# Kernel tuning notes

Hardware: AMD Instinct MI355X
Metric: run time of the kernel (lower is better)

The kernel has to match this reference:

```python
import jax, jax.numpy as jnp
import numpy as np

N_NODES = 100000
N_EDGES = 1600000
IN_F = 64
HID = 64
OUT_F = 64


def _param(key, shape, fan_in):
    return jax.random.normal(key, shape, dtype=jnp.float32) * (1.0 / np.sqrt(fan_in))


def setup_inputs() -> dict:
    key = jax.random.key(0)
    ks = jax.random.split(key, 12)
    features = jax.random.normal(ks[0], (N_NODES, IN_F), dtype=jnp.float32)
    src = jax.random.randint(ks[1], (N_EDGES,), 0, N_NODES, dtype=jnp.int32)
    dst = jax.random.randint(ks[2], (N_EDGES,), 0, N_NODES, dtype=jnp.int32)
    dims = [(IN_F, HID), (HID, HID), (HID, OUT_F)]
    inp = {"features": features, "src": src, "dst": dst}
    for i, (din, dout) in enumerate(dims):
        inp[f"W_self{i}"] = _param(ks[3 + 3 * i], (din, dout), din)
        inp[f"W_neigh{i}"] = _param(ks[4 + 3 * i], (din, dout), din)
        inp[f"b{i}"] = jnp.zeros((dout,), dtype=jnp.float32)
    return inp


def _sage_layer(h, src, dst, W_self, W_neigh, b, deg_inv, n_nodes, act):
    # mean aggregation over in-neighbors: gather src feats, segment-sum into dst
    msum = jax.ops.segment_sum(h[src], dst, num_segments=n_nodes)  # [N, d]
    h_neigh = msum * deg_inv  # mean (zero-degree nodes -> 0, matching DGL)
    out = h @ W_self + h_neigh @ W_neigh + b
    return jax.nn.relu(out) if act else out


def reference(features, src, dst, W_self0, W_neigh0, b0, W_self1, W_neigh1, b1, W_self2, W_neigh2, b2):
    n = features.shape[0]
    deg = jax.ops.segment_sum(jnp.ones((src.shape[0],), jnp.float32), dst, num_segments=n)
    deg_inv = (1.0 / jnp.maximum(deg, 1.0))[:, None]  # [N, 1]
    h = _sage_layer(features, src, dst, W_self0, W_neigh0, b0, deg_inv, n, act=True)
    h = _sage_layer(h, src, dst, W_self1, W_neigh1, b1, deg_inv, n, act=True)
    h = _sage_layer(h, src, dst, W_self2, W_neigh2, b2, deg_inv, n, act=False)
    return h
```

## Files before the change

### kernel.cpp

```cpp
#include <hip/hip_runtime.h>

#define NF 64
#define BUCKET 128
#define MAXB 8192
#define EPB 4096

typedef __attribute__((ext_vector_type(8))) short bf16x8;
typedef __attribute__((ext_vector_type(4))) float f32x4;
typedef __attribute__((ext_vector_type(4))) unsigned int u32x4;

__device__ __forceinline__ float bf2f(unsigned short x) {
    union { unsigned int u; float f; } v; v.u = ((unsigned int)x) << 16; return v.f;
}
__device__ __forceinline__ unsigned short f2bf(float x) {
    union { float f; unsigned int u; } v; v.f = x;
    unsigned int r = (v.u + 0x7FFFu + ((v.u >> 16) & 1u)) >> 16;
    return (unsigned short)r;
}


__global__ __launch_bounds__(256) void bhist_kernel(const int* __restrict__ dst,
                                                    int* __restrict__ bins,
                                                    int n_edges, int nb) {
    __shared__ int h[MAXB];
    for (int i = threadIdx.x; i < nb; i += 256) h[i] = 0;
    __syncthreads();
    int base = blockIdx.x * EPB;
    int lim = min(base + EPB, n_edges);
    for (int i = base + threadIdx.x; i < lim; i += 256)
        atomicAdd(&h[dst[i] >> 7], 1);
    __syncthreads();
    for (int i = threadIdx.x; i < nb; i += 256) {
        int v = h[i];
        if (v) atomicAdd(&bins[i], v);
    }
}

__global__ __launch_bounds__(1024) void bscan_kernel(const int* __restrict__ bins,
                                                     int* __restrict__ bptr,
                                                     int* __restrict__ gcur, int nb) {
    __shared__ int sd[1024];
    int carry = 0;
    if (threadIdx.x == 0) bptr[0] = 0;
    for (int base = 0; base < nb; base += 1024) {
        int i = base + threadIdx.x;
        int v = (i < nb) ? bins[i] : 0;
        sd[threadIdx.x] = v;
        __syncthreads();
        for (int off = 1; off < 1024; off <<= 1) {
            int t = (threadIdx.x >= off) ? sd[threadIdx.x - off] : 0;
            __syncthreads();
            sd[threadIdx.x] += t;
            __syncthreads();
        }
        if (i < nb) {
            int ex = carry + sd[threadIdx.x] - v;
            bptr[i + 1] = carry + sd[threadIdx.x];
            gcur[i] = ex;
        }
        int last = sd[1023];
        __syncthreads();
        carry += last;
    }
}

__global__ __launch_bounds__(256) void bscatter_kernel(const int* __restrict__ src,
                                                       const int* __restrict__ dst,
                                                       int* __restrict__ gcur,
                                                       unsigned* __restrict__ bedges,
                                                       int n_edges, int nb) {
    __shared__ int h[MAXB];
    for (int i = threadIdx.x; i < nb; i += 256) h[i] = 0;
    __syncthreads();
    int base = blockIdx.x * EPB;
    int myDst[16], mySrc[16];
#pragma unroll
    for (int k = 0; k < 16; ++k) {
        int i = base + k * 256 + threadIdx.x;
        if (i < n_edges) {
            myDst[k] = dst[i];
            mySrc[k] = src[i];
            atomicAdd(&h[myDst[k] >> 7], 1);
        } else {
            myDst[k] = -1;
        }
    }
    __syncthreads();
    for (int i = threadIdx.x; i < nb; i += 256) {
        int v = h[i];
        h[i] = v ? atomicAdd(&gcur[i], v) : 0;
    }
    __syncthreads();
#pragma unroll
    for (int k = 0; k < 16; ++k) {
        if (myDst[k] >= 0) {
            int bin = myDst[k] >> 7;
            int pos = atomicAdd(&h[bin], 1);
            bedges[pos] = ((unsigned)mySrc[k] << 7) | (unsigned)(myDst[k] & 127);
        }
    }
}

__global__ __launch_bounds__(256) void bfinal_kernel(
    const unsigned* __restrict__ bedges, const int* __restrict__ bptr,
    int* __restrict__ row_ptr, int* __restrict__ col,
    int n_nodes, int n_edges, int nb) {
    __shared__ int cnt[BUCKET];
    __shared__ int sa[BUCKET], sb2[BUCKET];
    int tid = threadIdx.x;
    int b = blockIdx.x;
    int beg = bptr[b], end = bptr[b + 1];
    if (tid < BUCKET) cnt[tid] = 0;
    __syncthreads();
    for (int i = beg + tid; i < end; i += 256)
        atomicAdd(&cnt[bedges[i] & (BUCKET - 1)], 1);
    __syncthreads();
    if (tid < BUCKET) sa[tid] = cnt[tid];
    __syncthreads();
    int* pin = sa; int* pout = sb2;
    for (int off = 1; off < BUCKET; off <<= 1) {
        if (tid < BUCKET) pout[tid] = pin[tid] + ((tid >= off) ? pin[tid - off] : 0);
        __syncthreads();
        int* t = pin; pin = pout; pout = t;
    }
    int nodeBase = b * BUCKET;
    if (tid < BUCKET && nodeBase + tid < n_nodes)
        row_ptr[nodeBase + tid] = beg + (tid ? pin[tid - 1] : 0);
    if (b == nb - 1 && tid == 0) row_ptr[n_nodes] = n_edges;
    __syncthreads();
    if (tid < BUCKET) cnt[tid] = 0;
    __syncthreads();
    for (int i = beg + tid; i < end; i += 256) {
        unsigned e = bedges[i];
        int d = e & (BUCKET - 1);
        int pos = beg + (d ? pin[d - 1] : 0) + atomicAdd(&cnt[d], 1);
        col[pos] = (int)(e >> 7);
    }
}


__global__ void convert_kernel(const float* __restrict__ in, unsigned short* __restrict__ X, int n_nodes) {
    int t = blockIdx.x * blockDim.x + threadIdx.x;
    int total = n_nodes * 16;
    if (t >= total) return;
    int n = t >> 4, g = t & 15;
    float4 v = *reinterpret_cast<const float4*>(in + (size_t)n * 64 + g * 4);
    ushort4 o;
    o.x = f2bf(v.x); o.y = f2bf(v.y); o.z = f2bf(v.z); o.w = f2bf(v.w);
    *reinterpret_cast<ushort4*>(X + (size_t)n * 128 + g * 4) = o;
}

__global__ void wtrans_kernel(const float* __restrict__ Ws0, const float* __restrict__ Wn0,
                              const float* __restrict__ Ws1, const float* __restrict__ Wn1,
                              const float* __restrict__ Ws2, const float* __restrict__ Wn2,
                              unsigned short* __restrict__ WT) {
    int t = blockIdx.x * blockDim.x + threadIdx.x;
    if (t >= 3 * 64 * 128) return;
    int layer = t >> 13;
    int r = t & 8191;
    int j = r >> 7, k = r & 127;
    const float* Ws = layer == 0 ? Ws0 : (layer == 1 ? Ws1 : Ws2);
    const float* Wn = layer == 0 ? Wn0 : (layer == 1 ? Wn1 : Wn2);
    float v = (k < 64) ? Ws[k * 64 + j] : Wn[(k - 64) * 64 + j];
    WT[t] = f2bf(v);
}

__global__ __launch_bounds__(256) void aggregate_bf16_kernel(
    unsigned short* __restrict__ X, const int* __restrict__ row_ptr, const int* __restrict__ col,
    int n_nodes) {
    int lane = threadIdx.x & 63;
    int wid = threadIdx.x >> 6;
    int q = lane >> 3;
    int j = lane & 7;
    int n = blockIdx.x * 4 + wid;
    if (n >= n_nodes) return;
    int beg = row_ptr[n], end = row_ptr[n + 1];
    float a[8] = {0.f, 0.f, 0.f, 0.f, 0.f, 0.f, 0.f, 0.f};
    for (int i = beg; i < end; i += 16) {
        int e0 = i + q, e1 = i + 8 + q;
        bool ok0 = e0 < end, ok1 = e1 < end;
        int s0 = col[ok0 ? e0 : end - 1];
        int s1 = col[ok1 ? e1 : end - 1];
        u32x4 v0 = *reinterpret_cast<const u32x4*>(X + (size_t)s0 * 128 + j * 8);
        u32x4 v1 = *reinterpret_cast<const u32x4*>(X + (size_t)s1 * 128 + j * 8);
        if (ok0) {
#pragma unroll
            for (int k = 0; k < 4; ++k) {
                union { unsigned u; float f; } lo, hi;
                lo.u = v0[k] << 16; hi.u = v0[k] & 0xffff0000u;
                a[2 * k] += lo.f; a[2 * k + 1] += hi.f;
            }
        }
        if (ok1) {
#pragma unroll
            for (int k = 0; k < 4; ++k) {
                union { unsigned u; float f; } lo, hi;
                lo.u = v1[k] << 16; hi.u = v1[k] & 0xffff0000u;
                a[2 * k] += lo.f; a[2 * k + 1] += hi.f;
            }
        }
    }
#pragma unroll
    for (int k = 0; k < 8; ++k) {
        a[k] += __shfl_xor(a[k], 8);
        a[k] += __shfl_xor(a[k], 16);
        a[k] += __shfl_xor(a[k], 32);
    }
    if (q == 0) {
        float dinv = 1.0f / fmaxf((float)(end - beg), 1.0f);
        u32x4 o;
#pragma unroll
        for (int k = 0; k < 4; ++k)
            o[k] = ((unsigned)f2bf(a[2 * k + 1] * dinv) << 16) | f2bf(a[2 * k] * dinv);
        *reinterpret_cast<u32x4*>(X + (size_t)n * 128 + 64 + j * 8) = o;
    }
}

__global__ __launch_bounds__(256) void linear_mfma_kernel(
    const unsigned short* __restrict__ X, const unsigned short* __restrict__ WT,
    const float* __restrict__ bias, unsigned short* __restrict__ outBf,
    float* __restrict__ outF32, int n_nodes, int do_relu) {
    int lane = threadIdx.x & 63;
    int wid = threadIdx.x >> 6;
    int l15 = lane & 15;
    int lg = lane >> 4;

    bf16x8 wf[4][4];
#pragma unroll
    for (int ft = 0; ft < 4; ++ft)
#pragma unroll
        for (int ks = 0; ks < 4; ++ks)
            wf[ft][ks] = *reinterpret_cast<const bf16x8*>(
                WT + (size_t)(ft * 16 + l15) * 128 + ks * 32 + lg * 8);

    float4 bv[4];
#pragma unroll
    for (int ft = 0; ft < 4; ++ft)
        bv[ft] = *reinterpret_cast<const float4*>(bias + ft * 16 + lg * 4);

    int tiles = (n_nodes + 15) >> 4;
    for (int tile = blockIdx.x * 4 + wid; tile < tiles; tile += gridDim.x * 4) {
        int nodeBase = tile * 16;
        int nrow = nodeBase + l15;
        int rrow = nrow < n_nodes ? nrow : n_nodes - 1;

        bf16x8 xf[4];
#pragma unroll
        for (int ks = 0; ks < 4; ++ks)
            xf[ks] = *reinterpret_cast<const bf16x8*>(X + (size_t)rrow * 128 + ks * 32 + lg * 8);

        f32x4 acc[4];
#pragma unroll
        for (int ft = 0; ft < 4; ++ft) acc[ft] = (f32x4){0.f, 0.f, 0.f, 0.f};
#pragma unroll
        for (int ks = 0; ks < 4; ++ks) {
#pragma unroll
            for (int ft = 0; ft < 4; ++ft)
                acc[ft] = __builtin_amdgcn_mfma_f32_16x16x32_bf16(wf[ft][ks], xf[ks], acc[ft], 0, 0, 0);
        }

        if (nrow < n_nodes) {
#pragma unroll
            for (int ft = 0; ft < 4; ++ft) {
                float4 v;
                v.x = acc[ft][0] + bv[ft].x;
                v.y = acc[ft][1] + bv[ft].y;
                v.z = acc[ft][2] + bv[ft].z;
                v.w = acc[ft][3] + bv[ft].w;
                if (do_relu) {
                    v.x = fmaxf(v.x, 0.f); v.y = fmaxf(v.y, 0.f);
                    v.z = fmaxf(v.z, 0.f); v.w = fmaxf(v.w, 0.f);
                }
                int fbase = ft * 16 + lg * 4;
                if (outF32) {
                    *reinterpret_cast<float4*>(outF32 + (size_t)nrow * 64 + fbase) = v;
                } else {
                    ushort4 o;
                    o.x = f2bf(v.x); o.y = f2bf(v.y); o.z = f2bf(v.z); o.w = f2bf(v.w);
                    *reinterpret_cast<ushort4*>(outBf + (size_t)nrow * 128 + fbase) = o;
                }
            }
        }
    }
}


__global__ void deg_kernel(const int* __restrict__ dst, float* __restrict__ deg, int n_edges) {
    int e = blockIdx.x * blockDim.x + threadIdx.x;
    if (e < n_edges) unsafeAtomicAdd(&deg[dst[e]], 1.0f);
}

__global__ void inv_kernel(float* __restrict__ deg, int n) {
    int i = blockIdx.x * blockDim.x + threadIdx.x;
    if (i < n) deg[i] = 1.0f / fmaxf(deg[i], 1.0f);
}

__global__ __launch_bounds__(256) void scatter_kernel(
    const float* __restrict__ h, const int* __restrict__ src, const int* __restrict__ dst,
    float* __restrict__ agg, int n_edges) {
    int t = blockIdx.x * blockDim.x + threadIdx.x;
    int e = t >> 4;
    if (e >= n_edges) return;
    int q = (t & 15) * 4;
    int s = src[e];
    int d = dst[e];
    float4 v = *reinterpret_cast<const float4*>(h + (size_t)s * NF + q);
    float* o = agg + (size_t)d * NF + q;
    unsafeAtomicAdd(o + 0, v.x);
    unsafeAtomicAdd(o + 1, v.y);
    unsafeAtomicAdd(o + 2, v.z);
    unsafeAtomicAdd(o + 3, v.w);
}

__global__ __launch_bounds__(256) void linear_kernel(
    const float* __restrict__ h, const float* __restrict__ agg, const float* __restrict__ deginv,
    const float* __restrict__ Ws, const float* __restrict__ Wn, const float* __restrict__ bias,
    float* __restrict__ out, int n_nodes, int do_relu) {
    __shared__ float sWs[NF * NF];
    __shared__ float sWn[NF * NF];
    __shared__ float sb[NF];
    for (int i = threadIdx.x; i < NF * NF; i += 256) {
        sWs[i] = Ws[i];
        sWn[i] = Wn[i];
    }
    if (threadIdx.x < NF) sb[threadIdx.x] = bias[threadIdx.x];
    __syncthreads();
    int j = threadIdx.x & 63;
    int sub = threadIdx.x >> 6;
    for (int n = blockIdx.x * 4 + sub; n < n_nodes; n += gridDim.x * 4) {
        const float4* hr = reinterpret_cast<const float4*>(h + (size_t)n * NF);
        const float4* ar = reinterpret_cast<const float4*>(agg + (size_t)n * NF);
        float accS = 0.f, accN = 0.f;
#pragma unroll
        for (int k4 = 0; k4 < 16; ++k4) {
            float4 hv = hr[k4];
            float4 av = ar[k4];
            int kb = k4 * 4;
            accS += hv.x * sWs[(kb + 0) * NF + j];
            accN += av.x * sWn[(kb + 0) * NF + j];
            accS += hv.y * sWs[(kb + 1) * NF + j];
            accN += av.y * sWn[(kb + 1) * NF + j];
            accS += hv.z * sWs[(kb + 2) * NF + j];
            accN += av.z * sWn[(kb + 2) * NF + j];
            accS += hv.w * sWs[(kb + 3) * NF + j];
            accN += av.w * sWn[(kb + 3) * NF + j];
        }
        float val = accS + deginv[n] * accN + sb[j];
        if (do_relu) val = fmaxf(val, 0.f);
        out[(size_t)n * NF + j] = val;
    }
}


extern "C" void kernel_launch(void* const* d_in, const int* in_sizes, int n_in,
                              void* d_out, int out_size, void* d_ws, size_t ws_size,
                              hipStream_t stream) {
    const float* features = (const float*)d_in[0];
    const int* src = (const int*)d_in[1];
    const int* dst = (const int*)d_in[2];
    const float* Ws0 = (const float*)d_in[3];
    const float* Wn0 = (const float*)d_in[4];
    const float* b0  = (const float*)d_in[5];
    const float* Ws1 = (const float*)d_in[6];
    const float* Wn1 = (const float*)d_in[7];
    const float* b1  = (const float*)d_in[8];
    const float* Ws2 = (const float*)d_in[9];
    const float* Wn2 = (const float*)d_in[10];
    const float* b2  = (const float*)d_in[11];

    const int n_nodes = in_sizes[0] / NF;
    const int n_edges = in_sizes[1];
    float* out = (float*)d_out;

    const int nb = (n_nodes + BUCKET - 1) / BUCKET;
    const size_t alignNB = (((size_t)nb + 1) * 4 + 255) / 256 * 256;
    const size_t alignN = (((size_t)n_nodes + 64) * 4 + 255) / 256 * 256;
    const size_t alignE = ((size_t)n_edges * 4 + 255) / 256 * 256;
    const size_t xBytes = ((size_t)n_nodes * 128 * 2 + 255) / 256 * 256;
    const size_t wtBytes = 3 * 64 * 128 * 2;

    dim3 blk(256);
    const int nEB = (n_edges + EPB - 1) / EPB;
    const int waveBlocks = (n_nodes + 3) / 4;
    const int tiles = (n_nodes + 15) / 16;
    const int linBlocks = (tiles + 3) / 4;

    const size_t need = 3 * alignNB + alignN + alignE + 2 * xBytes + wtBytes;
    const bool outFits = (size_t)out_size * sizeof(float) >= (size_t)n_edges * sizeof(unsigned);

    if (ws_size >= need && nb <= MAXB && n_nodes < (1 << 25) && outFits) {
        char* ws = (char*)d_ws;
        int* bins     = (int*)ws;
        int* bptr     = (int*)(ws + alignNB);
        int* gcur     = (int*)(ws + 2 * alignNB);
        int* row_ptr  = (int*)(ws + 3 * alignNB);
        int* col      = (int*)(ws + 3 * alignNB + alignN);
        unsigned short* X0  = (unsigned short*)(ws + 3 * alignNB + alignN + alignE);
        unsigned short* X1  = (unsigned short*)((char*)X0 + xBytes);
        unsigned short* WT  = (unsigned short*)((char*)X1 + xBytes);
        unsigned short* WT0 = WT;
        unsigned short* WT1 = WT + 64 * 128;
        unsigned short* WT2 = WT + 2 * 64 * 128;
        unsigned* bedges = (unsigned*)d_out;

        hipMemsetAsync(bins, 0, (size_t)nb * sizeof(int), stream);
        bhist_kernel<<<nEB, blk, 0, stream>>>(dst, bins, n_edges, nb);
        bscan_kernel<<<1, 1024, 0, stream>>>(bins, bptr, gcur, nb);
        bscatter_kernel<<<nEB, blk, 0, stream>>>(src, dst, gcur, bedges, n_edges, nb);
        bfinal_kernel<<<nb, blk, 0, stream>>>(bedges, bptr, row_ptr, col, n_nodes, n_edges, nb);

        convert_kernel<<<(n_nodes * 16 + 255) / 256, blk, 0, stream>>>(features, X0, n_nodes);
        wtrans_kernel<<<96, blk, 0, stream>>>(Ws0, Wn0, Ws1, Wn1, Ws2, Wn2, WT);

        aggregate_bf16_kernel<<<waveBlocks, blk, 0, stream>>>(X0, row_ptr, col, n_nodes);
        linear_mfma_kernel<<<linBlocks, blk, 0, stream>>>(X0, WT0, b0, X1, nullptr, n_nodes, 1);
        aggregate_bf16_kernel<<<waveBlocks, blk, 0, stream>>>(X1, row_ptr, col, n_nodes);
        linear_mfma_kernel<<<linBlocks, blk, 0, stream>>>(X1, WT1, b1, X0, nullptr, n_nodes, 1);
        aggregate_bf16_kernel<<<waveBlocks, blk, 0, stream>>>(X0, row_ptr, col, n_nodes);
        linear_mfma_kernel<<<linBlocks, blk, 0, stream>>>(X0, WT2, b2, nullptr, out, n_nodes, 0);
    } else {
        char* ws = (char*)d_ws;
        size_t degBytes = (((size_t)n_nodes * 4) + 255) / 256 * 256;
        float* deg = (float*)ws;
        float* agg = (float*)(ws + degBytes);
        float* h1  = agg + (size_t)n_nodes * NF;
        int scatBlocks = (n_edges * 16 + 255) / 256;
        int eBlocks = (n_edges + 255) / 256;
        size_t rowBytes = (size_t)n_nodes * NF * sizeof(float);

        hipMemsetAsync(deg, 0, (size_t)n_nodes * sizeof(float), stream);
        deg_kernel<<<eBlocks, blk, 0, stream>>>(dst, deg, n_edges);
        inv_kernel<<<(n_nodes + 255) / 256, blk, 0, stream>>>(deg, n_nodes);

        hipMemsetAsync(agg, 0, rowBytes, stream);
        scatter_kernel<<<scatBlocks, blk, 0, stream>>>(features, src, dst, agg, n_edges);
        linear_kernel<<<waveBlocks, blk, 0, stream>>>(features, agg, deg, Ws0, Wn0, b0, out, n_nodes, 1);

        hipMemsetAsync(agg, 0, rowBytes, stream);
        scatter_kernel<<<scatBlocks, blk, 0, stream>>>(out, src, dst, agg, n_edges);
        linear_kernel<<<waveBlocks, blk, 0, stream>>>(out, agg, deg, Ws1, Wn1, b1, h1, n_nodes, 1);

        hipMemsetAsync(agg, 0, rowBytes, stream);
        scatter_kernel<<<scatBlocks, blk, 0, stream>>>(h1, src, dst, agg, n_edges);
        linear_kernel<<<waveBlocks, blk, 0, stream>>>(h1, agg, deg, Ws2, Wn2, b2, out, n_nodes, 0);
    }
}
```

Measured before the change: 258.7 us.

## Fuse neighbor aggregation and MFMA linear into one per-layer kernel

Replaces the separate aggregate and linear kernels with one fused kernel per layer. Each 1024-thread block aggregates 16 nodes (one wave per node), stages the bf16 means in shared memory, and then four waves run the MFMA linear step for that tile. The node feature buffer shrinks from 128 to 64 bf16 per row, since the aggregated half no longer goes to global memory. This removes a global write and re-read of the aggregated features and three kernel launches. In exchange, the MFMA waves wait at a block barrier on the slowest node's aggregation, and 12 of 16 waves sit idle during the linear phase.

```diff
diff --git a/kernel.cpp b/kernel.cpp
--- a/kernel.cpp
+++ b/kernel.cpp
@@ -54,9 +54,8 @@
             __syncthreads();
         }
         if (i < nb) {
-            int ex = carry + sd[threadIdx.x] - v;
             bptr[i + 1] = carry + sd[threadIdx.x];
-            gcur[i] = ex;
+            gcur[i] = carry + sd[threadIdx.x] - v;
         }
         int last = sd[1023];
         __syncthreads();
@@ -147,7 +146,7 @@
     float4 v = *reinterpret_cast<const float4*>(in + (size_t)n * 64 + g * 4);
     ushort4 o;
     o.x = f2bf(v.x); o.y = f2bf(v.y); o.z = f2bf(v.z); o.w = f2bf(v.w);
-    *reinterpret_cast<ushort4*>(X + (size_t)n * 128 + g * 4) = o;
+    *reinterpret_cast<ushort4*>(X + (size_t)n * 64 + g * 4) = o;
 }
 
 __global__ void wtrans_kernel(const float* __restrict__ Ws0, const float* __restrict__ Wn0,
@@ -165,120 +164,111 @@
     WT[t] = f2bf(v);
 }
 
-__global__ __launch_bounds__(256) void aggregate_bf16_kernel(
-    unsigned short* __restrict__ X, const int* __restrict__ row_ptr, const int* __restrict__ col,
-    int n_nodes) {
-    int lane = threadIdx.x & 63;
-    int wid = threadIdx.x >> 6;
+__global__ __launch_bounds__(1024) void fused_layer_kernel(
+    const unsigned short* __restrict__ Xin,
+    const int* __restrict__ row_ptr, const int* __restrict__ col,
+    const unsigned short* __restrict__ WT,
+    const float* __restrict__ bias,
+    unsigned short* __restrict__ XoutBf,
+    float* __restrict__ outF32,
+    int n_nodes, int do_relu) {
+    __shared__ unsigned short aggT[16][72];
+    int tid = threadIdx.x;
+    int wid = tid >> 6;
+    int lane = tid & 63;
+    int nodeBase = blockIdx.x * 16;
+
+    int n = nodeBase + wid;
     int q = lane >> 3;
     int j = lane & 7;
-    int n = blockIdx.x * 4 + wid;
-    if (n >= n_nodes) return;
-    int beg = row_ptr[n], end = row_ptr[n + 1];
-    float a[8] = {0.f, 0.f, 0.f, 0.f, 0.f, 0.f, 0.f, 0.f};
-    for (int i = beg; i < end; i += 16) {
-        int e0 = i + q, e1 = i + 8 + q;
-        bool ok0 = e0 < end, ok1 = e1 < end;
-        int s0 = col[ok0 ? e0 : end - 1];
-        int s1 = col[ok1 ? e1 : end - 1];
-        u32x4 v0 = *reinterpret_cast<const u32x4*>(X + (size_t)s0 * 128 + j * 8);
-        u32x4 v1 = *reinterpret_cast<const u32x4*>(X + (size_t)s1 * 128 + j * 8);
-        if (ok0) {
-#pragma unroll
-            for (int k = 0; k < 4; ++k) {
-                union { unsigned u; float f; } lo, hi;
-                lo.u = v0[k] << 16; hi.u = v0[k] & 0xffff0000u;
-                a[2 * k] += lo.f; a[2 * k + 1] += hi.f;
+    if (n < n_nodes) {
+        int beg = row_ptr[n], end = row_ptr[n + 1];
+        float a[8] = {0.f, 0.f, 0.f, 0.f, 0.f, 0.f, 0.f, 0.f};
+        for (int i = beg; i < end; i += 16) {
+            int e0 = i + q, e1 = i + 8 + q;
+            bool ok0 = e0 < end, ok1 = e1 < end;
+            int s0 = col[ok0 ? e0 : end - 1];
+            int s1 = col[ok1 ? e1 : end - 1];
+            u32x4 v0 = *reinterpret_cast<const u32x4*>(Xin + (size_t)s0 * 64 + j * 8);
+            u32x4 v1 = *reinterpret_cast<const u32x4*>(Xin + (size_t)s1 * 64 + j * 8);
+            if (ok0) {
+#pragma unroll
+                for (int k = 0; k < 4; ++k) {
+                    union { unsigned u; float f; } lo, hi;
+                    lo.u = v0[k] << 16; hi.u = v0[k] & 0xffff0000u;
+                    a[2 * k] += lo.f; a[2 * k + 1] += hi.f;
+                }
             }
-        }
-        if (ok1) {
-#pragma unroll
-            for (int k = 0; k < 4; ++k) {
-                union { unsigned u; float f; } lo, hi;
-                lo.u = v1[k] << 16; hi.u = v1[k] & 0xffff0000u;
-                a[2 * k] += lo.f; a[2 * k + 1] += hi.f;
+            if (ok1) {
+#pragma unroll
+                for (int k = 0; k < 4; ++k) {
+                    union { unsigned u; float f; } lo, hi;
+                    lo.u = v1[k] << 16; hi.u = v1[k] & 0xffff0000u;
+                    a[2 * k] += lo.f; a[2 * k + 1] += hi.f;
+                }
             }
         }
-    }
-#pragma unroll
-    for (int k = 0; k < 8; ++k) {
-        a[k] += __shfl_xor(a[k], 8);
-        a[k] += __shfl_xor(a[k], 16);
-        a[k] += __shfl_xor(a[k], 32);
-    }
-    if (q == 0) {
-        float dinv = 1.0f / fmaxf((float)(end - beg), 1.0f);
-        u32x4 o;
-#pragma unroll
-        for (int k = 0; k < 4; ++k)
-            o[k] = ((unsigned)f2bf(a[2 * k + 1] * dinv) << 16) | f2bf(a[2 * k] * dinv);
-        *reinterpret_cast<u32x4*>(X + (size_t)n * 128 + 64 + j * 8) = o;
-    }
-}
-
-__global__ __launch_bounds__(256) void linear_mfma_kernel(
-    const unsigned short* __restrict__ X, const unsigned short* __restrict__ WT,
-    const float* __restrict__ bias, unsigned short* __restrict__ outBf,
-    float* __restrict__ outF32, int n_nodes, int do_relu) {
-    int lane = threadIdx.x & 63;
-    int wid = threadIdx.x >> 6;
-    int l15 = lane & 15;
-    int lg = lane >> 4;
-
-    bf16x8 wf[4][4];
-#pragma unroll
-    for (int ft = 0; ft < 4; ++ft)
+#pragma unroll
+        for (int k = 0; k < 8; ++k) {
+            a[k] += __shfl_xor(a[k], 8);
+            a[k] += __shfl_xor(a[k], 16);
+            a[k] += __shfl_xor(a[k], 32);
+        }
+        if (q == 0) {
+            float dinv = 1.0f / fmaxf((float)(end - beg), 1.0f);
+            u32x4 o;
+#pragma unroll
+            for (int k = 0; k < 4; ++k)
+                o[k] = ((unsigned)f2bf(a[2 * k + 1] * dinv) << 16) | f2bf(a[2 * k] * dinv);
+            *reinterpret_cast<u32x4*>(&aggT[wid][j * 8]) = o;
+        }
+    }
+    __syncthreads();
+
+    if (wid < 4) {
+        int ft = wid;
+        int l15 = lane & 15;
+        int lg = lane >> 4;
+
+        bf16x8 wf[4];
 #pragma unroll
         for (int ks = 0; ks < 4; ++ks)
-            wf[ft][ks] = *reinterpret_cast<const bf16x8*>(
+            wf[ks] = *reinterpret_cast<const bf16x8*>(
                 WT + (size_t)(ft * 16 + l15) * 128 + ks * 32 + lg * 8);
 
-    float4 bv[4];
-#pragma unroll
-    for (int ft = 0; ft < 4; ++ft)
-        bv[ft] = *reinterpret_cast<const float4*>(bias + ft * 16 + lg * 4);
-
-    int tiles = (n_nodes + 15) >> 4;
-    for (int tile = blockIdx.x * 4 + wid; tile < tiles; tile += gridDim.x * 4) {
-        int nodeBase = tile * 16;
+        float4 bv = *reinterpret_cast<const float4*>(bias + ft * 16 + lg * 4);
+
         int nrow = nodeBase + l15;
         int rrow = nrow < n_nodes ? nrow : n_nodes - 1;
 
         bf16x8 xf[4];
+        xf[0] = *reinterpret_cast<const bf16x8*>(Xin + (size_t)rrow * 64 + lg * 8);
+        xf[1] = *reinterpret_cast<const bf16x8*>(Xin + (size_t)rrow * 64 + 32 + lg * 8);
+        xf[2] = *reinterpret_cast<const bf16x8*>(&aggT[l15][lg * 8]);
+        xf[3] = *reinterpret_cast<const bf16x8*>(&aggT[l15][32 + lg * 8]);
+
+        f32x4 acc = (f32x4){0.f, 0.f, 0.f, 0.f};
 #pragma unroll
         for (int ks = 0; ks < 4; ++ks)
-            xf[ks] = *reinterpret_cast<const bf16x8*>(X + (size_t)rrow * 128 + ks * 32 + lg * 8);
-
-        f32x4 acc[4];
-#pragma unroll
-        for (int ft = 0; ft < 4; ++ft) acc[ft] = (f32x4){0.f, 0.f, 0.f, 0.f};
-#pragma unroll
-        for (int ks = 0; ks < 4; ++ks) {
-#pragma unroll
-            for (int ft = 0; ft < 4; ++ft)
-                acc[ft] = __builtin_amdgcn_mfma_f32_16x16x32_bf16(wf[ft][ks], xf[ks], acc[ft], 0, 0, 0);
-        }
+            acc = __builtin_amdgcn_mfma_f32_16x16x32_bf16(wf[ks], xf[ks], acc, 0, 0, 0);
 
         if (nrow < n_nodes) {
-#pragma unroll
-            for (int ft = 0; ft < 4; ++ft) {
-                float4 v;
-                v.x = acc[ft][0] + bv[ft].x;
-                v.y = acc[ft][1] + bv[ft].y;
-                v.z = acc[ft][2] + bv[ft].z;
-                v.w = acc[ft][3] + bv[ft].w;
-                if (do_relu) {
-                    v.x = fmaxf(v.x, 0.f); v.y = fmaxf(v.y, 0.f);
-                    v.z = fmaxf(v.z, 0.f); v.w = fmaxf(v.w, 0.f);
-                }
-                int fbase = ft * 16 + lg * 4;
-                if (outF32) {
-                    *reinterpret_cast<float4*>(outF32 + (size_t)nrow * 64 + fbase) = v;
-                } else {
-                    ushort4 o;
-                    o.x = f2bf(v.x); o.y = f2bf(v.y); o.z = f2bf(v.z); o.w = f2bf(v.w);
-                    *reinterpret_cast<ushort4*>(outBf + (size_t)nrow * 128 + fbase) = o;
-                }
+            float4 v;
+            v.x = acc[0] + bv.x;
+            v.y = acc[1] + bv.y;
+            v.z = acc[2] + bv.z;
+            v.w = acc[3] + bv.w;
+            if (do_relu) {
+                v.x = fmaxf(v.x, 0.f); v.y = fmaxf(v.y, 0.f);
+                v.z = fmaxf(v.z, 0.f); v.w = fmaxf(v.w, 0.f);
+            }
+            int fbase = ft * 16 + lg * 4;
+            if (outF32) {
+                *reinterpret_cast<float4*>(outF32 + (size_t)nrow * 64 + fbase) = v;
+            } else {
+                ushort4 o;
+                o.x = f2bf(v.x); o.y = f2bf(v.y); o.z = f2bf(v.z); o.w = f2bf(v.w);
+                *reinterpret_cast<ushort4*>(XoutBf + (size_t)nrow * 64 + fbase) = o;
             }
         }
     }
@@ -376,14 +366,12 @@
     const size_t alignNB = (((size_t)nb + 1) * 4 + 255) / 256 * 256;
     const size_t alignN = (((size_t)n_nodes + 64) * 4 + 255) / 256 * 256;
     const size_t alignE = ((size_t)n_edges * 4 + 255) / 256 * 256;
-    const size_t xBytes = ((size_t)n_nodes * 128 * 2 + 255) / 256 * 256;
+    const size_t xBytes = ((size_t)n_nodes * 64 * 2 + 255) / 256 * 256;
     const size_t wtBytes = 3 * 64 * 128 * 2;
 
     dim3 blk(256);
     const int nEB = (n_edges + EPB - 1) / EPB;
-    const int waveBlocks = (n_nodes + 3) / 4;
     const int tiles = (n_nodes + 15) / 16;
-    const int linBlocks = (tiles + 3) / 4;
 
     const size_t need = 3 * alignNB + alignN + alignE + 2 * xBytes + wtBytes;
     const bool outFits = (size_t)out_size * sizeof(float) >= (size_t)n_edges * sizeof(unsigned);
@@ -412,12 +400,9 @@
         convert_kernel<<<(n_nodes * 16 + 255) / 256, blk, 0, stream>>>(features, X0, n_nodes);
         wtrans_kernel<<<96, blk, 0, stream>>>(Ws0, Wn0, Ws1, Wn1, Ws2, Wn2, WT);
 
-        aggregate_bf16_kernel<<<waveBlocks, blk, 0, stream>>>(X0, row_ptr, col, n_nodes);
-        linear_mfma_kernel<<<linBlocks, blk, 0, stream>>>(X0, WT0, b0, X1, nullptr, n_nodes, 1);
-        aggregate_bf16_kernel<<<waveBlocks, blk, 0, stream>>>(X1, row_ptr, col, n_nodes);
-        linear_mfma_kernel<<<linBlocks, blk, 0, stream>>>(X1, WT1, b1, X0, nullptr, n_nodes, 1);
-        aggregate_bf16_kernel<<<waveBlocks, blk, 0, stream>>>(X0, row_ptr, col, n_nodes);
-        linear_mfma_kernel<<<linBlocks, blk, 0, stream>>>(X0, WT2, b2, nullptr, out, n_nodes, 0);
+        fused_layer_kernel<<<tiles, 1024, 0, stream>>>(X0, row_ptr, col, WT0, b0, X1, nullptr, n_nodes, 1);
+        fused_layer_kernel<<<tiles, 1024, 0, stream>>>(X1, row_ptr, col, WT1, b1, X0, nullptr, n_nodes, 1);
+        fused_layer_kernel<<<tiles, 1024, 0, stream>>>(X0, row_ptr, col, WT2, b2, nullptr, out, n_nodes, 0);
     } else {
         char* ws = (char*)d_ws;
         size_t degBytes = (((size_t)n_nodes * 4) + 255) / 256 * 256;
@@ -426,6 +411,7 @@
         float* h1  = agg + (size_t)n_nodes * NF;
         int scatBlocks = (n_edges * 16 + 255) / 256;
         int eBlocks = (n_edges + 255) / 256;
+        int waveBlocks = (n_nodes + 3) / 4;
         size_t rowBytes = (size_t)n_nodes * NF * sizeof(float);
 
         hipMemsetAsync(deg, 0, (size_t)n_nodes * sizeof(float), stream);
```

After: 272.9 us. +5.5%, slower.

## Slice features into 8-column planes for cache-friendly gather aggregation

Applied to the files above, without the earlier changes.

Node features move from an interleaved [N,128] self+aggregate row to eight planar slices of 8 bf16 columns, stored as separate X and aggregate buffers. Aggregation now runs one block set per slice, so each slice's gather set (about 1.6 MB) can stay in cache while irregular neighbour reads are served. The linear MFMA kernel reads from and writes to the planar layout. The bucket scatter also switches to larger per-block edge chunks and re-reads edges instead of holding them in registers; the cost is more blocks re-reading row_ptr and col per slice.

```diff
diff --git a/kernel.cpp b/kernel.cpp
--- a/kernel.cpp
+++ b/kernel.cpp
@@ -4,6 +4,7 @@
 #define BUCKET 128
 #define MAXB 8192
 #define EPB 4096
+#define SEPB 16384
 
 typedef __attribute__((ext_vector_type(8))) short bf16x8;
 typedef __attribute__((ext_vector_type(4))) float f32x4;
@@ -54,9 +55,8 @@
             __syncthreads();
         }
         if (i < nb) {
-            int ex = carry + sd[threadIdx.x] - v;
             bptr[i + 1] = carry + sd[threadIdx.x];
-            gcur[i] = ex;
+            gcur[i] = carry + sd[threadIdx.x] - v;
         }
         int last = sd[1023];
         __syncthreads();
@@ -72,32 +72,20 @@
     __shared__ int h[MAXB];
     for (int i = threadIdx.x; i < nb; i += 256) h[i] = 0;
     __syncthreads();
-    int base = blockIdx.x * EPB;
-    int myDst[16], mySrc[16];
-#pragma unroll
-    for (int k = 0; k < 16; ++k) {
-        int i = base + k * 256 + threadIdx.x;
-        if (i < n_edges) {
-            myDst[k] = dst[i];
-            mySrc[k] = src[i];
-            atomicAdd(&h[myDst[k] >> 7], 1);
-        } else {
-            myDst[k] = -1;
-        }
-    }
+    int base = blockIdx.x * SEPB;
+    int lim = min(base + SEPB, n_edges);
+    for (int i = base + threadIdx.x; i < lim; i += 256)
+        atomicAdd(&h[dst[i] >> 7], 1);
     __syncthreads();
     for (int i = threadIdx.x; i < nb; i += 256) {
         int v = h[i];
         h[i] = v ? atomicAdd(&gcur[i], v) : 0;
     }
     __syncthreads();
-#pragma unroll
-    for (int k = 0; k < 16; ++k) {
-        if (myDst[k] >= 0) {
-            int bin = myDst[k] >> 7;
-            int pos = atomicAdd(&h[bin], 1);
-            bedges[pos] = ((unsigned)mySrc[k] << 7) | (unsigned)(myDst[k] & 127);
-        }
+    for (int i = base + threadIdx.x; i < lim; i += 256) {
+        int d = dst[i];
+        int pos = atomicAdd(&h[d >> 7], 1);
+        bedges[pos] = ((unsigned)src[i] << 7) | (unsigned)(d & 127);
     }
 }
 
@@ -139,7 +127,7 @@
 }
 
 
-__global__ void convert_kernel(const float* __restrict__ in, unsigned short* __restrict__ X, int n_nodes) {
+__global__ void convert_kernel(const float* __restrict__ in, unsigned short* __restrict__ XP, int n_nodes) {
     int t = blockIdx.x * blockDim.x + threadIdx.x;
     int total = n_nodes * 16;
     if (t >= total) return;
@@ -147,7 +135,8 @@
     float4 v = *reinterpret_cast<const float4*>(in + (size_t)n * 64 + g * 4);
     ushort4 o;
     o.x = f2bf(v.x); o.y = f2bf(v.y); o.z = f2bf(v.z); o.w = f2bf(v.w);
-    *reinterpret_cast<ushort4*>(X + (size_t)n * 128 + g * 4) = o;
+    int p = g >> 1, off = (g & 1) * 4;
+    *reinterpret_cast<ushort4*>(XP + ((size_t)p * n_nodes + n) * 8 + off) = o;
 }
 
 __global__ void wtrans_kernel(const float* __restrict__ Ws0, const float* __restrict__ Wn0,
@@ -165,61 +154,59 @@
     WT[t] = f2bf(v);
 }
 
-__global__ __launch_bounds__(256) void aggregate_bf16_kernel(
-    unsigned short* __restrict__ X, const int* __restrict__ row_ptr, const int* __restrict__ col,
+__global__ __launch_bounds__(256) void aggregate_sliced_kernel(
+    const unsigned short* __restrict__ XP,
+    unsigned short* __restrict__ AP,
+    const int* __restrict__ row_ptr, const int* __restrict__ col,
     int n_nodes) {
-    int lane = threadIdx.x & 63;
-    int wid = threadIdx.x >> 6;
-    int q = lane >> 3;
-    int j = lane & 7;
-    int n = blockIdx.x * 4 + wid;
+    int s = blockIdx.x & 7;
+    int group = blockIdx.x >> 3;
+    int tid = threadIdx.x;
+    int wid = tid >> 6;
+    int lane = tid & 63;
+    int sub = lane >> 4;
+    int slot = lane & 15;
+    int n = group * 16 + wid * 4 + sub;
     if (n >= n_nodes) return;
     int beg = row_ptr[n], end = row_ptr[n + 1];
+    const unsigned short* plane = XP + (size_t)s * n_nodes * 8;
+
     float a[8] = {0.f, 0.f, 0.f, 0.f, 0.f, 0.f, 0.f, 0.f};
-    for (int i = beg; i < end; i += 16) {
-        int e0 = i + q, e1 = i + 8 + q;
-        bool ok0 = e0 < end, ok1 = e1 < end;
-        int s0 = col[ok0 ? e0 : end - 1];
-        int s1 = col[ok1 ? e1 : end - 1];
-        u32x4 v0 = *reinterpret_cast<const u32x4*>(X + (size_t)s0 * 128 + j * 8);
-        u32x4 v1 = *reinterpret_cast<const u32x4*>(X + (size_t)s1 * 128 + j * 8);
-        if (ok0) {
-#pragma unroll
-            for (int k = 0; k < 4; ++k) {
-                union { unsigned u; float f; } lo, hi;
-                lo.u = v0[k] << 16; hi.u = v0[k] & 0xffff0000u;
-                a[2 * k] += lo.f; a[2 * k + 1] += hi.f;
-            }
-        }
-        if (ok1) {
-#pragma unroll
-            for (int k = 0; k < 4; ++k) {
-                union { unsigned u; float f; } lo, hi;
-                lo.u = v1[k] << 16; hi.u = v1[k] & 0xffff0000u;
-                a[2 * k] += lo.f; a[2 * k + 1] += hi.f;
-            }
+    for (int i = beg + slot; i < end; i += 16) {
+        int sidx = __builtin_nontemporal_load(col + i);
+        u32x4 v = *reinterpret_cast<const u32x4*>(plane + (size_t)sidx * 8);
+#pragma unroll
+        for (int k = 0; k < 4; ++k) {
+            union { unsigned u; float f; } lo, hi;
+            lo.u = v[k] << 16; hi.u = v[k] & 0xffff0000u;
+            a[2 * k] += lo.f; a[2 * k + 1] += hi.f;
         }
     }
 #pragma unroll
     for (int k = 0; k < 8; ++k) {
+        a[k] += __shfl_xor(a[k], 1);
+        a[k] += __shfl_xor(a[k], 2);
+        a[k] += __shfl_xor(a[k], 4);
         a[k] += __shfl_xor(a[k], 8);
-        a[k] += __shfl_xor(a[k], 16);
-        a[k] += __shfl_xor(a[k], 32);
-    }
-    if (q == 0) {
+    }
+    if (slot == 0) {
         float dinv = 1.0f / fmaxf((float)(end - beg), 1.0f);
         u32x4 o;
 #pragma unroll
         for (int k = 0; k < 4; ++k)
             o[k] = ((unsigned)f2bf(a[2 * k + 1] * dinv) << 16) | f2bf(a[2 * k] * dinv);
-        *reinterpret_cast<u32x4*>(X + (size_t)n * 128 + 64 + j * 8) = o;
+        *reinterpret_cast<u32x4*>(AP + ((size_t)s * n_nodes + n) * 8) = o;
     }
 }
 
 __global__ __launch_bounds__(256) void linear_mfma_kernel(
-    const unsigned short* __restrict__ X, const unsigned short* __restrict__ WT,
-    const float* __restrict__ bias, unsigned short* __restrict__ outBf,
-    float* __restrict__ outF32, int n_nodes, int do_relu) {
+    const unsigned short* __restrict__ XP,
+    const unsigned short* __restrict__ AP,
+    const unsigned short* __restrict__ WT,
+    const float* __restrict__ bias,
+    unsigned short* __restrict__ XPout,
+    float* __restrict__ outF32,
+    int n_nodes, int do_relu) {
     int lane = threadIdx.x & 63;
     int wid = threadIdx.x >> 6;
     int l15 = lane & 15;
@@ -245,9 +232,10 @@
         int rrow = nrow < n_nodes ? nrow : n_nodes - 1;
 
         bf16x8 xf[4];
-#pragma unroll
-        for (int ks = 0; ks < 4; ++ks)
-            xf[ks] = *reinterpret_cast<const bf16x8*>(X + (size_t)rrow * 128 + ks * 32 + lg * 8);
+        xf[0] = *reinterpret_cast<const bf16x8*>(XP + ((size_t)(lg)     * n_nodes + rrow) * 8);
+        xf[1] = *reinterpret_cast<const bf16x8*>(XP + ((size_t)(4 + lg) * n_nodes + rrow) * 8);
+        xf[2] = *reinterpret_cast<const bf16x8*>(AP + ((size_t)(lg)     * n_nodes + rrow) * 8);
+        xf[3] = *reinterpret_cast<const bf16x8*>(AP + ((size_t)(4 + lg) * n_nodes + rrow) * 8);
 
         f32x4 acc[4];
 #pragma unroll
@@ -277,7 +265,8 @@
                 } else {
                     ushort4 o;
                     o.x = f2bf(v.x); o.y = f2bf(v.y); o.z = f2bf(v.z); o.w = f2bf(v.w);
-                    *reinterpret_cast<ushort4*>(outBf + (size_t)nrow * 128 + fbase) = o;
+                    int p = 2 * ft + (lg >> 1), off = (lg & 1) * 4;
+                    *reinterpret_cast<ushort4*>(XPout + ((size_t)p * n_nodes + nrow) * 8 + off) = o;
                 }
             }
         }
@@ -376,16 +365,17 @@
     const size_t alignNB = (((size_t)nb + 1) * 4 + 255) / 256 * 256;
     const size_t alignN = (((size_t)n_nodes + 64) * 4 + 255) / 256 * 256;
     const size_t alignE = ((size_t)n_edges * 4 + 255) / 256 * 256;
-    const size_t xBytes = ((size_t)n_nodes * 128 * 2 + 255) / 256 * 256;
+    const size_t xBytes = ((size_t)n_nodes * 64 * 2 + 255) / 256 * 256;
     const size_t wtBytes = 3 * 64 * 128 * 2;
 
     dim3 blk(256);
     const int nEB = (n_edges + EPB - 1) / EPB;
-    const int waveBlocks = (n_nodes + 3) / 4;
+    const int nSB = (n_edges + SEPB - 1) / SEPB;
     const int tiles = (n_nodes + 15) / 16;
     const int linBlocks = (tiles + 3) / 4;
-
-    const size_t need = 3 * alignNB + alignN + alignE + 2 * xBytes + wtBytes;
+    const int aggBlocks = 8 * ((n_nodes + 15) / 16);
+
+    const size_t need = 3 * alignNB + alignN + alignE + 3 * xBytes + wtBytes;
     const bool outFits = (size_t)out_size * sizeof(float) >= (size_t)n_edges * sizeof(unsigned);
 
     if (ws_size >= need && nb <= MAXB && n_nodes < (1 << 25) && outFits) {
@@ -395,9 +385,10 @@
         int* gcur     = (int*)(ws + 2 * alignNB);
         int* row_ptr  = (int*)(ws + 3 * alignNB);
         int* col      = (int*)(ws + 3 * alignNB + alignN);
-        unsigned short* X0  = (unsigned short*)(ws + 3 * alignNB + alignN + alignE);
-        unsigned short* X1  = (unsigned short*)((char*)X0 + xBytes);
-        unsigned short* WT  = (unsigned short*)((char*)X1 + xBytes);
+        unsigned short* XP0 = (unsigned short*)(ws + 3 * alignNB + alignN + alignE);
+        unsigned short* XP1 = (unsigned short*)((char*)XP0 + xBytes);
+        unsigned short* AP  = (unsigned short*)((char*)XP1 + xBytes);
+        unsigned short* WT  = (unsigned short*)((char*)AP + xBytes);
         unsigned short* WT0 = WT;
         unsigned short* WT1 = WT + 64 * 128;
         unsigned short* WT2 = WT + 2 * 64 * 128;
@@ -406,18 +397,18 @@
         hipMemsetAsync(bins, 0, (size_t)nb * sizeof(int), stream);
         bhist_kernel<<<nEB, blk, 0, stream>>>(dst, bins, n_edges, nb);
         bscan_kernel<<<1, 1024, 0, stream>>>(bins, bptr, gcur, nb);
-        bscatter_kernel<<<nEB, blk, 0, stream>>>(src, dst, gcur, bedges, n_edges, nb);
+        bscatter_kernel<<<nSB, blk, 0, stream>>>(src, dst, gcur, bedges, n_edges, nb);
         bfinal_kernel<<<nb, blk, 0, stream>>>(bedges, bptr, row_ptr, col, n_nodes, n_edges, nb);
 
-        convert_kernel<<<(n_nodes * 16 + 255) / 256, blk, 0, stream>>>(features, X0, n_nodes);
+        convert_kernel<<<(n_nodes * 16 + 255) / 256, blk, 0, stream>>>(features, XP0, n_nodes);
         wtrans_kernel<<<96, blk, 0, stream>>>(Ws0, Wn0, Ws1, Wn1, Ws2, Wn2, WT);
 
-        aggregate_bf16_kernel<<<waveBlocks, blk, 0, stream>>>(X0, row_ptr, col, n_nodes);
-        linear_mfma_kernel<<<linBlocks, blk, 0, stream>>>(X0, WT0, b0, X1, nullptr, n_nodes, 1);
-        aggregate_bf16_kernel<<<waveBlocks, blk, 0, stream>>>(X1, row_ptr, col, n_nodes);
-        linear_mfma_kernel<<<linBlocks, blk, 0, stream>>>(X1, WT1, b1, X0, nullptr, n_nodes, 1);
-        aggregate_bf16_kernel<<<waveBlocks, blk, 0, stream>>>(X0, row_ptr, col, n_nodes);
-        linear_mfma_kernel<<<linBlocks, blk, 0, stream>>>(X0, WT2, b2, nullptr, out, n_nodes, 0);
+        aggregate_sliced_kernel<<<aggBlocks, blk, 0, stream>>>(XP0, AP, row_ptr, col, n_nodes);
+        linear_mfma_kernel<<<linBlocks, blk, 0, stream>>>(XP0, AP, WT0, b0, XP1, nullptr, n_nodes, 1);
+        aggregate_sliced_kernel<<<aggBlocks, blk, 0, stream>>>(XP1, AP, row_ptr, col, n_nodes);
+        linear_mfma_kernel<<<linBlocks, blk, 0, stream>>>(XP1, AP, WT1, b1, XP0, nullptr, n_nodes, 1);
+        aggregate_sliced_kernel<<<aggBlocks, blk, 0, stream>>>(XP0, AP, row_ptr, col, n_nodes);
+        linear_mfma_kernel<<<linBlocks, blk, 0, stream>>>(XP0, AP, WT2, b2, nullptr, out, n_nodes, 0);
     } else {
         char* ws = (char*)d_ws;
         size_t degBytes = (((size_t)n_nodes * 4) + 255) / 256 * 256;
@@ -426,6 +417,7 @@
         float* h1  = agg + (size_t)n_nodes * NF;
         int scatBlocks = (n_edges * 16 + 255) / 256;
         int eBlocks = (n_edges + 255) / 256;
+        int waveBlocks = (n_nodes + 3) / 4;
         size_t rowBytes = (size_t)n_nodes * NF * sizeof(float);
 
         hipMemsetAsync(deg, 0, (size_t)n_nodes * sizeof(float), stream);
```

New measurement: 443.5 us. 71.4% more time.
